# Kernel tuning notes

Measured on AMD Instinct MI355X. Metric: run time of the kernel, lower is better.

## Reference

```python
import jax, jax.numpy as jnp
import numpy as np

B, S, D, DOM, L = 16, 512, 512, 8, 3  # batch, seq_len, mem_dim (S==D required by outputs*rel), domains, layers


def setup_inputs() -> dict:
    key = jax.random.key(0)
    ks = jax.random.split(key, 16)
    adj = jax.random.uniform(ks[0], (B, S, S), jnp.float32)
    rel = jax.random.uniform(ks[1], (B, S, S), jnp.float32)
    gcn_inputs = jax.random.normal(ks[2], (B, S, D), jnp.float32)
    frontrel = jax.random.normal(ks[3], (B, S, D), jnp.float32)
    backrel = jax.random.normal(ks[4], (B, S, D), jnp.float32)
    # depmap: exactly one selected column per (b, row) so masked_select reshapes to [B,S]
    depmap = jax.nn.one_hot(jax.random.randint(ks[5], (B, S), 0, S), S, dtype=jnp.float32)
    dom_idx = jax.random.randint(ks[6], (B, S), 0, DOM)
    has_dom = jax.random.bernoulli(ks[7], 0.5, (B, S)).astype(jnp.float32)
    domain_id = jax.nn.one_hot(dom_idx, DOM, dtype=jnp.float32) * has_dom[..., None]
    redom_idx = jax.random.randint(ks[8], (B, S), 0, DOM)
    has_re = jax.random.bernoulli(ks[9], 0.5, (B, S)).astype(jnp.float32)
    redomain_id = jax.nn.one_hot(redom_idx, DOM, dtype=jnp.float32) * has_re[..., None]
    domain = jax.random.bernoulli(ks[10], 0.5, (B, S, DOM, 1))
    mask = jnp.ones((B, S), dtype=bool)
    sc = 1.0 / np.sqrt(D)
    W_layers = jax.random.normal(ks[11], (L, D, D), jnp.float32) * sc
    b_layers = jnp.zeros((L, D), jnp.float32)
    prelu_a = jnp.full((L,), 0.25, jnp.float32)  # nn.PReLU default
    W_dg = jax.random.normal(ks[12], (D, D), jnp.float32) * sc
    b_dg = jnp.zeros((D,), jnp.float32)
    W_mg = jax.random.normal(ks[13], (2 * D, D), jnp.float32) * (1.0 / np.sqrt(2 * D))
    b_mg = jnp.zeros((D,), jnp.float32)
    W_out = jax.random.normal(ks[14], (L * D, D), jnp.float32) * (1.0 / np.sqrt(L * D))
    b_out = jnp.zeros((D,), jnp.float32)
    return dict(adj=adj, domain=domain, domain_id=domain_id, redomain_id=redomain_id,
                frontrel=frontrel, backrel=backrel, depmap=depmap, rel=rel,
                gcn_inputs=gcn_inputs, mask=mask, W_layers=W_layers, b_layers=b_layers,
                prelu_a=prelu_a, W_dg=W_dg, b_dg=b_dg, W_mg=W_mg, b_mg=b_mg,
                W_out=W_out, b_out=b_out)


def _forward(adj, domain, domain_id, redomain_id, frontrel, backrel, depmap, rel,
             gcn_inputs, W_layers, b_layers, prelu_a, W_dg, b_dg, W_mg, b_mg, W_out, b_out):
    denom = jnp.sum(adj, axis=2, keepdims=True) + 1.0                     # [B,S,1]
    domain_mask = jnp.sum(domain_id, axis=-1, keepdims=True) == 1.0       # [B,S,1]
    redomain_mask = jnp.sum(redomain_id, axis=-1, keepdims=True) == 1.0   # [B,S,1]
    frontadj = jnp.sum(adj * depmap, axis=-1)                             # [B,S]
    backadj = jnp.sum(jnp.swapaxes(adj, -1, -2) * depmap, axis=-1)        # [B,S]
    outputs = gcn_inputs
    outs = []
    for l in range(L):
        frontoutputs = jnp.where(domain_mask, 0.0, outputs)
        backoutputs = jnp.where(redomain_mask, 0.0, jnp.einsum('bij,bjd->bid', rel, outputs))
        # domain pooling: mask then max over sequence -> [B,DOM,D]
        pooled = jnp.max(jnp.where(domain, -10000.0, outputs[:, :, None, :]), axis=1)
        domain_outputs = jax.nn.sigmoid(pooled @ W_dg + b_dg)             # domain_gate
        frontoutputs = frontoutputs + jnp.einsum('bsk,bkd->bsd', domain_id, domain_outputs)
        backoutputs = backoutputs + jnp.einsum('bsk,bkd->bsd', redomain_id, domain_outputs)
        frontdepadj = jax.nn.sigmoid(jnp.concatenate([frontoutputs, frontrel], -1) @ W_mg + b_mg)
        backdepadj = jax.nn.sigmoid(jnp.concatenate([backoutputs, backrel], -1) @ W_mg + b_mg)
        delta = jnp.einsum('bji,bjd->bid', rel, frontadj[..., None] * frontdepadj * frontoutputs)
        delta = delta + backadj[..., None] * backdepadj * backoutputs
        Ax = jnp.einsum('bij,bjd->bid', adj, outputs * rel)               # requires S==D
        AxW = (Ax @ W_layers[l] + b_layers[l]) + (outputs @ W_layers[l] + b_layers[l]) + delta
        x = AxW / denom
        outputs = jnp.where(x >= 0, x, prelu_a[l] * x)                    # PReLU
        outs.append(outputs)                                              # dropout is eval-mode identity
    gcn_outputs = jnp.concatenate(outs, axis=2)                           # [B,S,L*D]
    return gcn_outputs @ W_out + b_out + gcn_inputs


def reference(adj, domain, domain_id, redomain_id, frontrel, backrel, depmap, rel,
              gcn_inputs, mask, W_layers, b_layers, prelu_a, W_dg, b_dg, W_mg, b_mg,
              W_out, b_out):
    return _forward(adj, domain, domain_id, redomain_id, frontrel, backrel, depmap, rel,
                    gcn_inputs, W_layers, b_layers, prelu_a, W_dg, b_dg, W_mg, b_mg,
                    W_out, b_out)
```

## Files before the change

### kernel.cpp

```cpp
#include <hip/hip_runtime.h>
#include <math.h>

#define SD_  (512*512)
#define BSD_ (16*512*512)

typedef unsigned short u16;
typedef short s16x8 __attribute__((ext_vector_type(8)));
typedef float f32x4 __attribute__((ext_vector_type(4)));

__device__ __forceinline__ float sigmoidf_(float x) { return 1.0f / (1.0f + __expf(-x)); }

__device__ __forceinline__ u16 f2bf(float f) {
    unsigned int u = __float_as_uint(f);
    u += 0x7fffu + ((u >> 16) & 1u);
    return (u16)(u >> 16);
}
__device__ __forceinline__ float bf2f(u16 h) { return __uint_as_float((unsigned)h << 16); }

__device__ __forceinline__ void glds16(const void* g, void* l) {
    __builtin_amdgcn_global_load_lds((const __attribute__((address_space(1))) unsigned int*)g,
                                     (__attribute__((address_space(3))) unsigned int*)l, 16, 0, 0);
}

struct GP {
    const u16 *A1, *A2;  int lda1, lda2;  long sA;
    const u16 *B1, *B2;  int ldb1, ldb2;  long sB;
    void *C1, *C2;  int obf1, obf2, ldc1, ldc2;  long sC;
    u16 *CT1, *CT2;  long sCT;
    const void *Ci1, *Ci2;  int cm1, cm2, ldci1, ldci2;  long sCi1, sCi2;
    const float *bias;  float bS;
    const float *sc1, *sc2;
    const int *selm1, *seli1, *selm2, *seli2;
    const float *DG;
    const float *invden, *prelu;  int pidx;
    int M, K, zs, swzX, swzY;
};

template<int EPI, int ASEL>
__global__ __launch_bounds__(512, 6)
void gemm3(const GP p)
{
    __shared__ short LS[24576];
    const int tid = threadIdx.x;
    int bx, by, bz;
    if (p.swzX >= 0) {
        const int bid = blockIdx.x + gridDim.x * (blockIdx.y + gridDim.y * blockIdx.z);
        const int ppx = (gridDim.y * gridDim.z) >> 3;
        const int xcd = bid & 7, idx = bid >> 3;
        const int pair = xcd * ppx + (idx >> p.swzX);
        bx = idx & ((1 << p.swzX) - 1);
        by = pair & ((1 << p.swzY) - 1);
        bz = pair >> p.swzY;
    } else { bx = blockIdx.x; by = blockIdx.y; bz = blockIdx.z; }

    const int seg = (bz >= p.zs) ? 1 : 0;
    const int z = seg ? bz - p.zs : bz;
    const u16* Ab = (seg ? p.A2 : p.A1) + z * p.sA;
    const int lda = seg ? p.lda2 : p.lda1;
    const u16* Bb = (seg ? p.B2 : p.B1) + z * p.sB;
    const int ldb = seg ? p.ldb2 : p.ldb1;

    const int m0 = by * 128, n0 = bx * 64;
    const int srow = ((tid >> 6) << 4) | (tid & 15);
    const int sk0 = ((tid >> 4) & 3) << 3;
    const bool doB = tid < 256;

    const u16* aRow = Ab + (long)(m0 + srow) * lda + sk0;
    const u16* bRow = Bb + (long)(n0 + srow) * ldb + sk0;

    int aselv = 0; long dgo = 0;
    if (ASEL) {
        const int* selm = seg ? p.selm2 : p.selm1;
        const int* seli = seg ? p.seli2 : p.seli1;
        const int r0 = m0 + srow;
        aselv = selm[r0];
        dgo = (long)(((r0 >> 9) << 3) + seli[r0]) * 512 + sk0;
    }

    auto stage = [&](int kk, int buf) {
        short* base = &LS[buf * 6144];
        if (ASEL) {
            s16x8 v;
            if (aselv) {
                const float* dg = p.DG + dgo + kk;
#pragma unroll
                for (int q = 0; q < 8; ++q) v[q] = (short)f2bf(dg[q]);
            } else v = *(const s16x8*)(aRow + kk);
            *(s16x8*)&base[tid * 8] = v;
        } else {
            glds16(aRow + kk, &base[tid * 8]);
        }
        if (doB) glds16(bRow + kk, &base[4096 + tid * 8]);
    };

    const int wave = tid >> 6, lane = tid & 63;
    const int gA = (wave >> 1) << 1;
    const int gB = (wave & 1) << 1;

    f32x4 acc[2][2] = {};
    const int nkb = p.K >> 5;
    stage(0, 0);
    stage(32, 1);
    for (int kb = 0; kb < nkb; ++kb) {
        if (kb + 2 < nkb) stage((kb + 2) << 5, (kb + 2) & 3);
        const int ahead = (nkb - 1 - kb) < 2 ? (nkb - 1 - kb) : 2;
        if (ASEL) {
            if (doB) {
                if (ahead == 2)      asm volatile("s_waitcnt vmcnt(2)" ::: "memory");
                else if (ahead == 1) asm volatile("s_waitcnt vmcnt(1)" ::: "memory");
                else                 asm volatile("s_waitcnt vmcnt(0)" ::: "memory");
            } else {
                asm volatile("s_waitcnt vmcnt(0)" ::: "memory");
            }
            asm volatile("s_waitcnt lgkmcnt(0)" ::: "memory");
        } else {
            if (doB) {
                if (ahead == 2)      asm volatile("s_waitcnt vmcnt(4)" ::: "memory");
                else if (ahead == 1) asm volatile("s_waitcnt vmcnt(2)" ::: "memory");
                else                 asm volatile("s_waitcnt vmcnt(0)" ::: "memory");
            } else {
                if (ahead == 2)      asm volatile("s_waitcnt vmcnt(2)" ::: "memory");
                else if (ahead == 1) asm volatile("s_waitcnt vmcnt(1)" ::: "memory");
                else                 asm volatile("s_waitcnt vmcnt(0)" ::: "memory");
            }
        }
        __builtin_amdgcn_s_barrier();
        const short* ls = &LS[(kb & 3) * 6144];
        s16x8 aF[2], bF[2];
#pragma unroll
        for (int mt = 0; mt < 2; ++mt) aF[mt] = *(const s16x8*)&ls[((gA + mt) * 64 + lane) * 8];
#pragma unroll
        for (int nt = 0; nt < 2; ++nt) bF[nt] = *(const s16x8*)&ls[4096 + ((gB + nt) * 64 + lane) * 8];
#pragma unroll
        for (int mt = 0; mt < 2; ++mt)
#pragma unroll
            for (int nt = 0; nt < 2; ++nt)
                acc[mt][nt] = __builtin_amdgcn_mfma_f32_16x16x32_bf16(aF[mt], bF[nt], acc[mt][nt], 0, 0, 0);
    }

    const int ml = lane & 15, quad = lane >> 4;
    const int wm = (wave >> 1) * 32, wn = (wave & 1) * 32;
    u16* Cb16 = (u16*)(seg ? p.C2 : p.C1);
    float* Cb32 = (float*)(seg ? p.C2 : p.C1);
    const int haveC = (seg ? p.C2 : p.C1) != nullptr;
    const int obf = seg ? p.obf2 : p.obf1;
    const int ldc = seg ? p.ldc2 : p.ldc1;
    if (haveC) { if (obf) Cb16 += z * p.sC; else Cb32 += z * p.sC; }
    u16* CTb = seg ? p.CT2 : p.CT1;
    if (CTb) CTb += z * p.sCT;
    const u16* CiT = (const u16*)(seg ? p.Ci2 : p.Ci1);
    const float* Ci32 = (const float*)(seg ? p.Ci2 : p.Ci1);
    const int cm = seg ? p.cm2 : p.cm1;
    const int ldci = seg ? p.ldci2 : p.ldci1;
    {
        const long sCi = seg ? p.sCi2 : p.sCi1;
        if (cm) CiT += z * sCi; else Ci32 += z * sCi;
    }
    const float pal = (EPI == 4) ? p.prelu[p.pidx] : 0.0f;
    const float* scp = (EPI == 8) ? (seg ? p.sc2 : p.sc1) : nullptr;
    const int* eselm = (EPI == 8) ? (seg ? p.selm2 : p.selm1) : nullptr;
    const int* eseli2 = (EPI == 8) ? (seg ? p.seli2 : p.seli1) : nullptr;

    const bool useEp = haveC && (obf == 1);
    u16* epbuf = (u16*)LS;
    if (useEp) __syncthreads();

#pragma unroll
    for (int mt = 0; mt < 2; ++mt) {
#pragma unroll
        for (int nt = 0; nt < 2; ++nt) {
            const int col = n0 + wn + nt * 16 + ml;
            const int rowb = m0 + wm + mt * 16 + quad * 4;
            float cin4[4];
            if (EPI == 3 || EPI == 4 || EPI == 7 || EPI == 8) {
                if (cm) {
                    const ushort4 c4 = *(const ushort4*)&CiT[(long)(rowb >> 9) * SD_ + (long)col * 512 + (rowb & 511)];
                    cin4[0] = bf2f(c4.x); cin4[1] = bf2f(c4.y); cin4[2] = bf2f(c4.z); cin4[3] = bf2f(c4.w);
                } else {
#pragma unroll
                    for (int r = 0; r < 4; ++r) cin4[r] = Ci32[(long)(rowb + r) * ldci + col];
                }
            }
            u16 pk[4];
#pragma unroll
            for (int r = 0; r < 4; ++r) {
                const int row = rowb + r;
                float x = acc[mt][nt][r];
                if (EPI == 1) x += p.bias[col];
                else if (EPI == 3) x += cin4[r];
                else if (EPI == 4) {
                    x = (x + p.bS * p.bias[col] + cin4[r]) * p.invden[z * p.M + row];
                    x = (x >= 0.0f) ? x : pal * x;
                }
                else if (EPI == 6) x = sigmoidf_(x + p.bias[col]);
                else if (EPI == 7) x += p.bias[col] + cin4[r];
                else if (EPI == 8) {
                    float av;
                    if (eselm[row]) av = p.DG[(long)(((row >> 9) << 3) + eseli2[row]) * 512 + col];
                    else av = bf2f(Ab[(long)row * lda + col]);
                    x = sigmoidf_(x + cin4[r]) * scp[row] * av;
                }
                if (haveC && obf == 0) Cb32[(long)row * ldc + col] = x;
                pk[r] = f2bf(x);
                if (useEp) epbuf[(wm + mt * 16 + quad * 4 + r) * 72 + wn + nt * 16 + ml] = pk[r];
            }
            if (CTb) {
                u16* ct = CTb + (long)(rowb >> 9) * SD_ + (long)col * 512 + (rowb & 511);
                *(ushort4*)ct = *(ushort4*)pk;
            }
        }
    }
    if (useEp) {
        __syncthreads();
        const int lr = tid >> 2, cs = (tid & 3) * 16;
#pragma unroll
        for (int j = 0; j < 2; ++j) {
            const s16x8 v = *(const s16x8*)&epbuf[lr * 72 + cs + j * 8];
            *(s16x8*)&Cb16[(long)(m0 + lr) * ldc + n0 + cs + j * 8] = v;
        }
    }
}

__global__ __launch_bounds__(256)
void cvt_k(const float* __restrict__ s, u16* __restrict__ d)
{
    const long i = ((long)blockIdx.x * 256 + threadIdx.x) * 4;
    const float4 v = *(const float4*)&s[i];
    ushort4 h = { f2bf(v.x), f2bf(v.y), f2bf(v.z), f2bf(v.w) };
    *(ushort4*)&d[i] = h;
}

__global__ __launch_bounds__(256)
void trcvt_k(const float* __restrict__ src, u16* __restrict__ dstT, u16* __restrict__ dstN,
             const int R, const int C, const long sS, const long sDT, const long sDN)
{
    __shared__ u16 t[64][72];
    const float* s = src + blockIdx.z * sS;
    const int r0 = blockIdx.y * 64, c0 = blockIdx.x * 64;
    const int tid = threadIdx.x;
    const int lr = tid >> 2, lc4 = (tid & 3) * 16;
#pragma unroll
    for (int j = 0; j < 4; ++j) {
        const float4 v = *(const float4*)&s[(long)(r0 + lr) * C + c0 + lc4 + j * 4];
        ushort4 h = { f2bf(v.x), f2bf(v.y), f2bf(v.z), f2bf(v.w) };
        *(ushort4*)&t[lr][lc4 + j * 4] = h;
        if (dstN) *(ushort4*)&dstN[blockIdx.z * sDN + (long)(r0 + lr) * C + c0 + lc4 + j * 4] = h;
    }
    __syncthreads();
    const int lcol = tid >> 2, rc = (tid & 3) * 16;
#pragma unroll
    for (int j = 0; j < 2; ++j) {
        s16x8 v;
#pragma unroll
        for (int q = 0; q < 8; ++q) v[q] = (short)t[rc + j * 8 + q][lcol];
        *(s16x8*)&dstT[blockIdx.z * sDT + (long)(c0 + lcol) * R + r0 + rc + j * 8] = v;
    }
}

__global__ __launch_bounds__(256)
void e0_k(const float* __restrict__ adj, const float* __restrict__ depmap,
          const float* __restrict__ domain_id, const float* __restrict__ redomain_id,
          float* __restrict__ invden, float* __restrict__ fa, int* __restrict__ dcol,
          int* __restrict__ dm, int* __restrict__ dsel, int* __restrict__ rm, int* __restrict__ rsel)
{
    const int bs = blockIdx.x;
    const int t = threadIdx.x;
    const float* arow = adj + (long)bs * 512;
    const float* drow = depmap + (long)bs * 512;
    __shared__ float red[256];
    __shared__ int scol;
    if (t == 0) scol = 0;
    const float a0 = arow[t], a1 = arow[t + 256];
    const float p0 = drow[t], p1 = drow[t + 256];
    if (p0 > 0.5f) scol = t;
    if (p1 > 0.5f) scol = t + 256;
    red[t] = a0 + a1;
    __syncthreads();
    for (int off = 128; off > 0; off >>= 1) { if (t < off) red[t] += red[t + off]; __syncthreads(); }
    if (t == 0) invden[bs] = 1.0f / (red[0] + 1.0f);
    __syncthreads();
    red[t] = a0 * p0 + a1 * p1;
    __syncthreads();
    for (int off = 128; off > 0; off >>= 1) { if (t < off) red[t] += red[t + off]; __syncthreads(); }
    if (t == 0) {
        fa[bs] = red[0];
        dcol[bs] = scol;
        const float* q = domain_id + (long)bs * 8;
        float s = 0.f; int sel = 0;
        for (int k = 0; k < 8; ++k) { float v = q[k]; s += v; if (v > 0.5f) sel = k; }
        dm[bs] = (s > 0.5f) ? 1 : 0; dsel[bs] = sel;
        const float* r = redomain_id + (long)bs * 8;
        s = 0.f; sel = 0;
        for (int k = 0; k < 8; ++k) { float v = r[k]; s += v; if (v > 0.5f) sel = k; }
        rm[bs] = (s > 0.5f) ? 1 : 0; rsel[bs] = sel;
    }
}

__global__ void e0b_k(const float* __restrict__ adj, const int* __restrict__ dcol, float* __restrict__ ba)
{
    const int bs = blockIdx.x * 256 + threadIdx.x;
    const int b = bs >> 9, s = bs & 511;
    ba[bs] = adj[((long)b * 512 + dcol[bs]) * 512 + s];
}

__global__ __launch_bounds__(256)
void pool1_k(const u16* __restrict__ OUT, const int ldO, const int* __restrict__ domain,
             const u16* __restrict__ relb, u16* __restrict__ cm, u16* __restrict__ OxRT)
{
    const int b = blockIdx.x >> 4, c = blockIdx.x & 15;
    const int s0 = c * 32, tid = threadIdx.x;
    __shared__ int dom[256];
    dom[tid] = domain[((long)(b * 512 + s0 + (tid >> 3))) * 8 + (tid & 7)];
    __syncthreads();
    const int d0 = tid * 2;
    float mxa[8], mxb[8];
#pragma unroll
    for (int k = 0; k < 8; ++k) { mxa[k] = -10000.0f; mxb[k] = -10000.0f; }
    s16x8 pA[4], pB[4];
#pragma unroll
    for (int s = 0; s < 32; ++s) {
        const int row = b * 512 + s0 + s;
        const unsigned uv = *(const unsigned*)&OUT[(long)row * ldO + d0];
        const unsigned rv = *(const unsigned*)&relb[(long)row * 512 + d0];
        const float vx = bf2f((u16)(uv & 0xffff)), vy = bf2f((u16)(uv >> 16));
        const float rx = bf2f((u16)(rv & 0xffff)), ry = bf2f((u16)(rv >> 16));
        pA[s >> 3][s & 7] = (short)f2bf(vx * rx);
        pB[s >> 3][s & 7] = (short)f2bf(vy * ry);
        const int* ds = &dom[s * 8];
#pragma unroll
        for (int k = 0; k < 8; ++k) {
            mxa[k] = fmaxf(mxa[k], ds[k] ? -10000.0f : vx);
            mxb[k] = fmaxf(mxb[k], ds[k] ? -10000.0f : vy);
        }
    }
#pragma unroll
    for (int j = 0; j < 4; ++j) *(s16x8*)&OxRT[((long)b * 512 + d0) * 512 + s0 + j * 8] = pA[j];
#pragma unroll
    for (int j = 0; j < 4; ++j) *(s16x8*)&OxRT[((long)b * 512 + d0 + 1) * 512 + s0 + j * 8] = pB[j];
#pragma unroll
    for (int k = 0; k < 8; ++k) {
        ushort2 h = { f2bf(mxa[k]), f2bf(mxb[k]) };
        *(ushort2*)&cm[((long)((b * 16 + c) * 8 + k)) * 512 + d0] = h;
    }
}

__global__ void pool2_k(const u16* __restrict__ cm, u16* __restrict__ pooled)
{
    const int q = blockIdx.x * 256 + threadIdx.x;
    const int b = q >> 12, k = (q >> 9) & 7, d = q & 511;
    float m = -1e30f;
    for (int c = 0; c < 16; ++c)
        m = fmaxf(m, bf2f(cm[((long)((b * 16 + c) * 8 + k)) * 512 + d]));
    pooled[((long)(b * 8 + k)) * 512 + d] = f2bf(m);
}

extern "C" void kernel_launch(void* const* d_in, const int* in_sizes, int n_in,
                              void* d_out, int out_size, void* d_ws, size_t ws_size,
                              hipStream_t stream)
{
    const float* adj         = (const float*)d_in[0];
    const int*   domain      = (const int*)d_in[1];
    const float* domain_id   = (const float*)d_in[2];
    const float* redomain_id = (const float*)d_in[3];
    const float* frontrel    = (const float*)d_in[4];
    const float* backrel     = (const float*)d_in[5];
    const float* depmap      = (const float*)d_in[6];
    const float* rel         = (const float*)d_in[7];
    const float* gcn         = (const float*)d_in[8];
    const float* W_layers    = (const float*)d_in[10];
    const float* b_layers    = (const float*)d_in[11];
    const float* prelu_a     = (const float*)d_in[12];
    const float* W_dg        = (const float*)d_in[13];
    const float* b_dg        = (const float*)d_in[14];
    const float* W_mg        = (const float*)d_in[15];
    const float* b_mg        = (const float*)d_in[16];
    const float* W_out       = (const float*)d_in[17];
    const float* b_out       = (const float*)d_in[18];
    float* out = (float*)d_out;

    char* w = (char*)d_ws;
    auto alloc = [&](size_t bytes) { void* p = (void*)w; w += (bytes + 255) & ~(size_t)255; return p; };
    const size_t Bb = (size_t)BSD_ * 2;
    u16* OUTS_bf = (u16*)alloc((size_t)8192 * 1536 * 2);
    u16* OUTT    = (u16*)alloc(Bb);
    u16* gcnT    = (u16*)alloc(Bb);
    u16* RB_bf   = (u16*)alloc(Bb);
    u16* XBT     = (u16*)alloc(Bb);
    u16* XFT     = (u16*)alloc(Bb);
    u16* OxRT    = (u16*)alloc(Bb);
    u16* DLT     = (u16*)alloc(Bb);
    u16* AXO_bf  = (u16*)alloc(Bb);
    u16* BBT     = (u16*)alloc(Bb);
    u16* FBT     = (u16*)alloc(Bb);
    u16* rel_bf  = (u16*)alloc(Bb);
    u16* relT_bf = (u16*)alloc(Bb);
    u16* adj_bf  = (u16*)alloc(Bb);
    u16* gcn_bf  = (u16*)alloc(Bb);
    u16* frel_bf = (u16*)alloc(Bb);
    u16* brel_bf = (u16*)alloc(Bb);
    u16* WmgT1 = (u16*)alloc((size_t)SD_ * 2);
    u16* WmgT2 = (u16*)alloc((size_t)SD_ * 2);
    u16* WdgT  = (u16*)alloc((size_t)SD_ * 2);
    u16* WlT   = (u16*)alloc((size_t)3 * SD_ * 2);
    u16* WoutT = (u16*)alloc((size_t)512 * 1536 * 2);
    u16* cm     = (u16*)alloc((size_t)16 * 16 * 8 * 512 * 2);
    u16* pooled = (u16*)alloc((size_t)16 * 8 * 512 * 2);
    float* DG     = (float*)alloc((size_t)16 * 8 * 512 * 4);
    float* invden = (float*)alloc(8192 * 4);
    float* fa     = (float*)alloc(8192 * 4);
    float* ba     = (float*)alloc(8192 * 4);
    int* dcol = (int*)alloc(8192 * 4);
    int* dm   = (int*)alloc(8192 * 4);
    int* dsel = (int*)alloc(8192 * 4);
    int* rm   = (int*)alloc(8192 * 4);
    int* rsel = (int*)alloc(8192 * 4);

    cvt_k<<<4096, 256, 0, stream>>>(adj, adj_bf);
    cvt_k<<<4096, 256, 0, stream>>>(frontrel, frel_bf);
    cvt_k<<<4096, 256, 0, stream>>>(backrel, brel_bf);
    trcvt_k<<<dim3(8, 8, 16), 256, 0, stream>>>(gcn, gcnT, gcn_bf, 512, 512, SD_, SD_, SD_);
    trcvt_k<<<dim3(8, 8, 16), 256, 0, stream>>>(rel, relT_bf, rel_bf, 512, 512, SD_, SD_, SD_);
    trcvt_k<<<dim3(8, 8, 1), 256, 0, stream>>>(W_mg, WmgT1, nullptr, 512, 512, 0, 0, 0);
    trcvt_k<<<dim3(8, 8, 1), 256, 0, stream>>>(W_mg + SD_, WmgT2, nullptr, 512, 512, 0, 0, 0);
    trcvt_k<<<dim3(8, 8, 1), 256, 0, stream>>>(W_dg, WdgT, nullptr, 512, 512, 0, 0, 0);
    trcvt_k<<<dim3(8, 8, 3), 256, 0, stream>>>(W_layers, WlT, nullptr, 512, 512, SD_, SD_, 0);
    trcvt_k<<<dim3(8, 24, 1), 256, 0, stream>>>(W_out, WoutT, nullptr, 1536, 512, 0, 0, 0);
    e0_k<<<8192, 256, 0, stream>>>(adj, depmap, domain_id, redomain_id, invden, fa, dcol, dm, dsel, rm, rsel);
    e0b_k<<<32, 256, 0, stream>>>(adj, dcol, ba);

    const dim3 blk(512);

    {
        GP p{};
        p.A1 = brel_bf; p.A2 = frel_bf; p.lda1 = p.lda2 = 512; p.sA = 0;
        p.B1 = p.B2 = WmgT2; p.ldb1 = p.ldb2 = 512; p.sB = 0;
        p.CT1 = BBT; p.CT2 = FBT; p.sCT = 0;
        p.bias = b_mg; p.M = 8192; p.K = 512; p.zs = 1; p.swzX = 3; p.swzY = 6;
        gemm3<1, 0><<<dim3(8, 64, 2), blk, 0, stream>>>(p);
    }

    for (int l = 0; l < 3; ++l) {
        const u16* OUTp  = (l == 0) ? gcn_bf : (OUTS_bf + (l - 1) * 512);
        const u16* OUTTp = (l == 0) ? gcnT : OUTT;
        const int ldO = (l == 0) ? 512 : 1536;

        {
            GP p{};
            p.A1 = rel_bf; p.lda1 = 512; p.sA = SD_;
            p.B1 = OUTTp; p.ldb1 = 512; p.sB = SD_;
            p.C1 = RB_bf; p.obf1 = 1; p.ldc1 = 512; p.sC = SD_;
            p.M = 512; p.K = 512; p.zs = 16; p.swzX = 3; p.swzY = 2;
            gemm3<0, 0><<<dim3(8, 4, 16), blk, 0, stream>>>(p);
        }
        pool1_k<<<256, 256, 0, stream>>>(OUTp, ldO, domain, rel_bf, cm, OxRT);
        pool2_k<<<256, 256, 0, stream>>>(cm, pooled);
        {
            GP p{};
            p.A1 = pooled; p.lda1 = 512; p.B1 = WdgT; p.ldb1 = 512;
            p.C1 = DG; p.obf1 = 0; p.ldc1 = 512;
            p.bias = b_dg; p.M = 128; p.K = 512; p.zs = 1; p.swzX = -1;
            gemm3<6, 0><<<dim3(8, 1, 1), blk, 0, stream>>>(p);
        }
        {
            GP p{};
            p.A1 = RB_bf; p.lda1 = 512; p.A2 = OUTp; p.lda2 = ldO; p.sA = 0;
            p.selm1 = rm; p.seli1 = rsel; p.selm2 = dm; p.seli2 = dsel; p.DG = DG;
            p.B1 = p.B2 = WmgT1; p.ldb1 = p.ldb2 = 512; p.sB = 0;
            p.Ci1 = BBT; p.Ci2 = FBT; p.cm1 = p.cm2 = 1; p.ldci1 = p.ldci2 = 512; p.sCi1 = p.sCi2 = 0;
            p.CT1 = XBT; p.CT2 = XFT; p.sCT = 0;
            p.sc1 = ba; p.sc2 = fa; p.M = 8192; p.K = 512; p.zs = 1; p.swzX = 3; p.swzY = 6;
            gemm3<8, 1><<<dim3(8, 64, 2), blk, 0, stream>>>(p);
        }
        {
            GP p{};
            p.A1 = relT_bf; p.lda1 = 512; p.A2 = adj_bf; p.lda2 = 512; p.sA = SD_;
            p.B1 = XFT; p.ldb1 = 512;
            p.B2 = OxRT; p.ldb2 = 512; p.sB = SD_;
            p.Ci1 = XBT; p.cm1 = 1; p.ldci1 = 512; p.sCi1 = SD_;
            p.Ci2 = OUTTp; p.cm2 = 1; p.ldci2 = 512; p.sCi2 = SD_;
            p.CT1 = DLT; p.sCT = SD_;
            p.C2 = AXO_bf; p.obf2 = 1; p.ldc2 = 512; p.sC = SD_;
            p.M = 512; p.K = 512; p.zs = 16; p.swzX = 3; p.swzY = 2;
            gemm3<3, 0><<<dim3(8, 4, 32), blk, 0, stream>>>(p);
        }
        {
            GP p{};
            p.A1 = AXO_bf; p.lda1 = 512; p.sA = SD_;
            p.B1 = WlT + (long)l * SD_; p.ldb1 = 512; p.sB = 0;
            p.Ci1 = DLT; p.cm1 = 1; p.ldci1 = 512; p.sCi1 = SD_;
            p.C1 = OUTS_bf + l * 512; p.obf1 = 1; p.ldc1 = 1536; p.sC = (long)512 * 1536;
            p.CT1 = OUTT; p.sCT = SD_;
            p.bias = b_layers + l * 512; p.bS = 2.0f;
            p.invden = invden; p.prelu = prelu_a; p.pidx = l;
            p.M = 512; p.K = 512; p.zs = 16; p.swzX = 3; p.swzY = 2;
            gemm3<4, 0><<<dim3(8, 4, 16), blk, 0, stream>>>(p);
        }
    }

    {
        GP p{};
        p.A1 = OUTS_bf; p.lda1 = 1536; p.sA = 0;
        p.B1 = WoutT; p.ldb1 = 1536; p.sB = 0;
        p.Ci1 = gcn; p.cm1 = 0; p.ldci1 = 512; p.sCi1 = 0;
        p.C1 = out; p.obf1 = 0; p.ldc1 = 512; p.sC = 0;
        p.bias = b_out; p.M = 8192; p.K = 1536; p.zs = 1; p.swzX = 3; p.swzY = 6;
        gemm3<7, 0><<<dim3(8, 64, 1), blk, 0, stream>>>(p);
    }
}
```

Before: 744.1 us.

## Double K-step per barrier with 3-buffer LDS pipeline in gemm3

The GEMM main loop now processes 64 K-elements per iteration instead of 32, using a 3-stage LDS ring of larger buffers. This halves the number of barriers and waitcnt syncs per tile. All 512 threads now share the B loads instead of only half. The ASEL path loads register data ahead of the barrier and writes it to LDS after, using vectorized float4 reads. In exchange, LDS use per block grows and the occupancy hint drops from 6 to 4 blocks.

```diff
diff --git a/kernel.cpp b/kernel.cpp
--- a/kernel.cpp
+++ b/kernel.cpp
@@ -37,10 +37,10 @@
 };
 
 template<int EPI, int ASEL>
-__global__ __launch_bounds__(512, 6)
+__global__ __launch_bounds__(512, 4)
 void gemm3(const GP p)
 {
-    __shared__ short LS[24576];
+    __shared__ short LS[36864];
     const int tid = threadIdx.x;
     int bx, by, bz;
     if (p.swzX >= 0) {
@@ -63,10 +63,12 @@
     const int m0 = by * 128, n0 = bx * 64;
     const int srow = ((tid >> 6) << 4) | (tid & 15);
     const int sk0 = ((tid >> 4) & 3) << 3;
-    const bool doB = tid < 256;
+    const int srB = (((tid >> 6) & 3) << 4) | (tid & 15);
+    const int skB = (((tid >> 4) & 3) << 3) | ((tid >> 8) << 5);
+    const int bslot = (tid & 255) * 8 + (tid >> 8) * 2048;
 
     const u16* aRow = Ab + (long)(m0 + srow) * lda + sk0;
-    const u16* bRow = Bb + (long)(n0 + srow) * ldb + sk0;
+    const u16* bRow = Bb + (long)(n0 + srB) * ldb + skB;
 
     int aselv = 0; long dgo = 0;
     if (ASEL) {
@@ -77,20 +79,26 @@
         dgo = (long)(((r0 >> 9) << 3) + seli[r0]) * 512 + sk0;
     }
 
-    auto stage = [&](int kk, int buf) {
-        short* base = &LS[buf * 6144];
-        if (ASEL) {
-            s16x8 v;
-            if (aselv) {
-                const float* dg = p.DG + dgo + kk;
-#pragma unroll
-                for (int q = 0; q < 8; ++q) v[q] = (short)f2bf(dg[q]);
-            } else v = *(const s16x8*)(aRow + kk);
-            *(s16x8*)&base[tid * 8] = v;
+    auto stageG = [&](int kb2) {
+        short* base = &LS[(kb2 % 3) * 12288];
+        const int kk = kb2 << 6;
+        glds16(aRow + kk,      &base[tid * 8]);
+        glds16(aRow + kk + 32, &base[4096 + tid * 8]);
+        glds16(bRow + kk,      &base[8192 + bslot]);
+    };
+    auto loadA = [&](int kb2, s16x8& a0, s16x8& a1) {
+        const int kk = kb2 << 6;
+        if (aselv) {
+            const float4* dg = (const float4*)(p.DG + dgo + kk);
+            const float4 d0 = dg[0], d1 = dg[1], d2 = dg[8], d3 = dg[9];
+            a0[0] = (short)f2bf(d0.x); a0[1] = (short)f2bf(d0.y); a0[2] = (short)f2bf(d0.z); a0[3] = (short)f2bf(d0.w);
+            a0[4] = (short)f2bf(d1.x); a0[5] = (short)f2bf(d1.y); a0[6] = (short)f2bf(d1.z); a0[7] = (short)f2bf(d1.w);
+            a1[0] = (short)f2bf(d2.x); a1[1] = (short)f2bf(d2.y); a1[2] = (short)f2bf(d2.z); a1[3] = (short)f2bf(d2.w);
+            a1[4] = (short)f2bf(d3.x); a1[5] = (short)f2bf(d3.y); a1[6] = (short)f2bf(d3.z); a1[7] = (short)f2bf(d3.w);
         } else {
-            glds16(aRow + kk, &base[tid * 8]);
-        }
-        if (doB) glds16(bRow + kk, &base[4096 + tid * 8]);
+            a0 = *(const s16x8*)(aRow + kk);
+            a1 = *(const s16x8*)(aRow + kk + 32);
+        }
     };
 
     const int wave = tid >> 6, lane = tid & 63;
@@ -98,44 +106,58 @@
     const int gB = (wave & 1) << 1;
 
     f32x4 acc[2][2] = {};
-    const int nkb = p.K >> 5;
-    stage(0, 0);
-    stage(32, 1);
+    const int nkb = p.K >> 6;
+
+    if (ASEL) {
+#pragma unroll
+        for (int s = 0; s < 2; ++s) {
+            s16x8 a0, a1;
+            loadA(s, a0, a1);
+            short* base = &LS[s * 12288];
+            *(s16x8*)&base[tid * 8] = a0;
+            *(s16x8*)&base[4096 + tid * 8] = a1;
+            glds16(bRow + (s << 6), &base[8192 + bslot]);
+        }
+    } else { stageG(0); stageG(1); }
+
     for (int kb = 0; kb < nkb; ++kb) {
-        if (kb + 2 < nkb) stage((kb + 2) << 5, (kb + 2) & 3);
-        const int ahead = (nkb - 1 - kb) < 2 ? (nkb - 1 - kb) : 2;
+        s16x8 nA0, nA1;
+        if (ASEL && kb + 2 < nkb) loadA(kb + 2, nA0, nA1);
+
         if (ASEL) {
-            if (doB) {
-                if (ahead == 2)      asm volatile("s_waitcnt vmcnt(2)" ::: "memory");
-                else if (ahead == 1) asm volatile("s_waitcnt vmcnt(1)" ::: "memory");
-                else                 asm volatile("s_waitcnt vmcnt(0)" ::: "memory");
-            } else {
-                asm volatile("s_waitcnt vmcnt(0)" ::: "memory");
-            }
+            if (kb + 2 < nkb)      asm volatile("s_waitcnt vmcnt(3)" ::: "memory");
+            else if (kb + 1 < nkb) asm volatile("s_waitcnt vmcnt(1)" ::: "memory");
+            else                   asm volatile("s_waitcnt vmcnt(0)" ::: "memory");
             asm volatile("s_waitcnt lgkmcnt(0)" ::: "memory");
         } else {
-            if (doB) {
-                if (ahead == 2)      asm volatile("s_waitcnt vmcnt(4)" ::: "memory");
-                else if (ahead == 1) asm volatile("s_waitcnt vmcnt(2)" ::: "memory");
-                else                 asm volatile("s_waitcnt vmcnt(0)" ::: "memory");
-            } else {
-                if (ahead == 2)      asm volatile("s_waitcnt vmcnt(2)" ::: "memory");
-                else if (ahead == 1) asm volatile("s_waitcnt vmcnt(1)" ::: "memory");
-                else                 asm volatile("s_waitcnt vmcnt(0)" ::: "memory");
-            }
+            if (kb + 1 < nkb)      asm volatile("s_waitcnt vmcnt(3)" ::: "memory");
+            else                   asm volatile("s_waitcnt vmcnt(0)" ::: "memory");
         }
         __builtin_amdgcn_s_barrier();
-        const short* ls = &LS[(kb & 3) * 6144];
-        s16x8 aF[2], bF[2];
-#pragma unroll
-        for (int mt = 0; mt < 2; ++mt) aF[mt] = *(const s16x8*)&ls[((gA + mt) * 64 + lane) * 8];
-#pragma unroll
-        for (int nt = 0; nt < 2; ++nt) bF[nt] = *(const s16x8*)&ls[4096 + ((gB + nt) * 64 + lane) * 8];
-#pragma unroll
-        for (int mt = 0; mt < 2; ++mt)
-#pragma unroll
-            for (int nt = 0; nt < 2; ++nt)
-                acc[mt][nt] = __builtin_amdgcn_mfma_f32_16x16x32_bf16(aF[mt], bF[nt], acc[mt][nt], 0, 0, 0);
+
+        if (kb + 2 < nkb) {
+            if (ASEL) {
+                short* base = &LS[((kb + 2) % 3) * 12288];
+                *(s16x8*)&base[tid * 8] = nA0;
+                *(s16x8*)&base[4096 + tid * 8] = nA1;
+                glds16(bRow + ((kb + 2) << 6), &base[8192 + bslot]);
+            } else stageG(kb + 2);
+        }
+
+        const short* ls = &LS[(kb % 3) * 12288];
+#pragma unroll
+        for (int kh = 0; kh < 2; ++kh) {
+            s16x8 aF[2], bF[2];
+#pragma unroll
+            for (int mt = 0; mt < 2; ++mt) aF[mt] = *(const s16x8*)&ls[kh * 4096 + ((gA + mt) * 64 + lane) * 8];
+#pragma unroll
+            for (int nt = 0; nt < 2; ++nt) bF[nt] = *(const s16x8*)&ls[8192 + kh * 2048 + ((gB + nt) * 64 + lane) * 8];
+#pragma unroll
+            for (int mt = 0; mt < 2; ++mt)
+#pragma unroll
+                for (int nt = 0; nt < 2; ++nt)
+                    acc[mt][nt] = __builtin_amdgcn_mfma_f32_16x16x32_bf16(aF[mt], bF[nt], acc[mt][nt], 0, 0, 0);
+        }
     }
 
     const int ml = lane & 15, quad = lane >> 4;
```

Measured after the change: 718.8 us. 3.4% less time.

## Load GEMM fragments directly from global into registers, drop LDS staging

Applied to the files above, without the earlier changes.

Replaces the LDS-staged, async global_load_lds pipeline in the shared GEMM kernel with direct per-lane global loads of MFMA fragments into registers, double-buffered across 64-wide k steps. It also stores the domain-gate result DG in bf16, so the selected-row A loads become plain vector loads without per-element conversion. LDS is kept only for the epilogue buffer, and launch bounds drop to 4 blocks per CU. Because A and B tiles are no longer shared through LDS, each wave reloads data from global/L2 that its neighbours also read, which raises memory traffic and register pressure in exchange for removing barriers and LDS round trips.

```diff
diff --git a/kernel.cpp b/kernel.cpp
--- a/kernel.cpp
+++ b/kernel.cpp
@@ -16,11 +16,6 @@
     return (u16)(u >> 16);
 }
 __device__ __forceinline__ float bf2f(u16 h) { return __uint_as_float((unsigned)h << 16); }
-
-__device__ __forceinline__ void glds16(const void* g, void* l) {
-    __builtin_amdgcn_global_load_lds((const __attribute__((address_space(1))) unsigned int*)g,
-                                     (__attribute__((address_space(3))) unsigned int*)l, 16, 0, 0);
-}
 
 struct GP {
     const u16 *A1, *A2;  int lda1, lda2;  long sA;
@@ -31,16 +26,16 @@
     const float *bias;  float bS;
     const float *sc1, *sc2;
     const int *selm1, *seli1, *selm2, *seli2;
-    const float *DG;
+    const u16 *DG;
     const float *invden, *prelu;  int pidx;
     int M, K, zs, swzX, swzY;
 };
 
 template<int EPI, int ASEL>
-__global__ __launch_bounds__(512, 6)
+__global__ __launch_bounds__(512, 4)
 void gemm3(const GP p)
 {
-    __shared__ short LS[24576];
+    __shared__ u16 epbuf[128 * 72];
     const int tid = threadIdx.x;
     int bx, by, bz;
     if (p.swzX >= 0) {
@@ -61,81 +56,61 @@
     const int ldb = seg ? p.ldb2 : p.ldb1;
 
     const int m0 = by * 128, n0 = bx * 64;
-    const int srow = ((tid >> 6) << 4) | (tid & 15);
-    const int sk0 = ((tid >> 4) & 3) << 3;
-    const bool doB = tid < 256;
-
-    const u16* aRow = Ab + (long)(m0 + srow) * lda + sk0;
-    const u16* bRow = Bb + (long)(n0 + srow) * ldb + sk0;
-
-    int aselv = 0; long dgo = 0;
-    if (ASEL) {
-        const int* selm = seg ? p.selm2 : p.selm1;
-        const int* seli = seg ? p.seli2 : p.seli1;
-        const int r0 = m0 + srow;
-        aselv = selm[r0];
-        dgo = (long)(((r0 >> 9) << 3) + seli[r0]) * 512 + sk0;
-    }
-
-    auto stage = [&](int kk, int buf) {
-        short* base = &LS[buf * 6144];
-        if (ASEL) {
-            s16x8 v;
-            if (aselv) {
-                const float* dg = p.DG + dgo + kk;
-#pragma unroll
-                for (int q = 0; q < 8; ++q) v[q] = (short)f2bf(dg[q]);
-            } else v = *(const s16x8*)(aRow + kk);
-            *(s16x8*)&base[tid * 8] = v;
-        } else {
-            glds16(aRow + kk, &base[tid * 8]);
-        }
-        if (doB) glds16(bRow + kk, &base[4096 + tid * 8]);
-    };
-
     const int wave = tid >> 6, lane = tid & 63;
     const int gA = (wave >> 1) << 1;
     const int gB = (wave & 1) << 1;
+    const int lr = lane & 15, lq = lane >> 4;
+
+    const u16* pAm[2];
+    const u16* pBn[2];
+#pragma unroll
+    for (int mt = 0; mt < 2; ++mt) {
+        const int row = m0 + (gA + mt) * 16 + lr;
+        const u16* base = Ab + (long)row * lda;
+        if (ASEL) {
+            const int* selm = seg ? p.selm2 : p.selm1;
+            const int* seli = seg ? p.seli2 : p.seli1;
+            if (selm[row]) base = p.DG + (long)(((row >> 9) << 3) + seli[row]) * 512;
+        }
+        pAm[mt] = base + lq * 8;
+    }
+#pragma unroll
+    for (int nt = 0; nt < 2; ++nt)
+        pBn[nt] = Bb + (long)(n0 + (gB + nt) * 16 + lr) * ldb + lq * 8;
 
     f32x4 acc[2][2] = {};
-    const int nkb = p.K >> 5;
-    stage(0, 0);
-    stage(32, 1);
-    for (int kb = 0; kb < nkb; ++kb) {
-        if (kb + 2 < nkb) stage((kb + 2) << 5, (kb + 2) & 3);
-        const int ahead = (nkb - 1 - kb) < 2 ? (nkb - 1 - kb) : 2;
-        if (ASEL) {
-            if (doB) {
-                if (ahead == 2)      asm volatile("s_waitcnt vmcnt(2)" ::: "memory");
-                else if (ahead == 1) asm volatile("s_waitcnt vmcnt(1)" ::: "memory");
-                else                 asm volatile("s_waitcnt vmcnt(0)" ::: "memory");
-            } else {
-                asm volatile("s_waitcnt vmcnt(0)" ::: "memory");
-            }
-            asm volatile("s_waitcnt lgkmcnt(0)" ::: "memory");
-        } else {
-            if (doB) {
-                if (ahead == 2)      asm volatile("s_waitcnt vmcnt(4)" ::: "memory");
-                else if (ahead == 1) asm volatile("s_waitcnt vmcnt(2)" ::: "memory");
-                else                 asm volatile("s_waitcnt vmcnt(0)" ::: "memory");
-            } else {
-                if (ahead == 2)      asm volatile("s_waitcnt vmcnt(2)" ::: "memory");
-                else if (ahead == 1) asm volatile("s_waitcnt vmcnt(1)" ::: "memory");
-                else                 asm volatile("s_waitcnt vmcnt(0)" ::: "memory");
-            }
-        }
-        __builtin_amdgcn_s_barrier();
-        const short* ls = &LS[(kb & 3) * 6144];
-        s16x8 aF[2], bF[2];
-#pragma unroll
-        for (int mt = 0; mt < 2; ++mt) aF[mt] = *(const s16x8*)&ls[((gA + mt) * 64 + lane) * 8];
-#pragma unroll
-        for (int nt = 0; nt < 2; ++nt) bF[nt] = *(const s16x8*)&ls[4096 + ((gB + nt) * 64 + lane) * 8];
-#pragma unroll
-        for (int mt = 0; mt < 2; ++mt)
-#pragma unroll
-            for (int nt = 0; nt < 2; ++nt)
-                acc[mt][nt] = __builtin_amdgcn_mfma_f32_16x16x32_bf16(aF[mt], bF[nt], acc[mt][nt], 0, 0, 0);
+
+    auto LD = [&](int kb, s16x8 (&A)[2][2], s16x8 (&B)[2][2]) {
+        const int ko = kb << 6;
+#pragma unroll
+        for (int mt = 0; mt < 2; ++mt) {
+            A[mt][0] = *(const s16x8*)(pAm[mt] + ko);
+            A[mt][1] = *(const s16x8*)(pAm[mt] + ko + 32);
+        }
+#pragma unroll
+        for (int nt = 0; nt < 2; ++nt) {
+            B[nt][0] = *(const s16x8*)(pBn[nt] + ko);
+            B[nt][1] = *(const s16x8*)(pBn[nt] + ko + 32);
+        }
+    };
+    auto MM = [&](const s16x8 (&A)[2][2], const s16x8 (&B)[2][2]) {
+#pragma unroll
+        for (int kh = 0; kh < 2; ++kh)
+#pragma unroll
+            for (int mt = 0; mt < 2; ++mt)
+#pragma unroll
+                for (int nt = 0; nt < 2; ++nt)
+                    acc[mt][nt] = __builtin_amdgcn_mfma_f32_16x16x32_bf16(A[mt][kh], B[nt][kh], acc[mt][nt], 0, 0, 0);
+    };
+
+    const int nkb = p.K >> 6;
+    s16x8 A0[2][2], B0[2][2], A1[2][2], B1[2][2];
+    LD(0, A0, B0);
+    for (int kb = 0; kb < nkb; kb += 2) {
+        LD(kb + 1, A1, B1);
+        MM(A0, B0);
+        if (kb + 2 < nkb) LD(kb + 2, A0, B0);
+        MM(A1, B1);
     }
 
     const int ml = lane & 15, quad = lane >> 4;
@@ -162,8 +137,6 @@
     const int* eseli2 = (EPI == 8) ? (seg ? p.seli2 : p.seli1) : nullptr;
 
     const bool useEp = haveC && (obf == 1);
-    u16* epbuf = (u16*)LS;
-    if (useEp) __syncthreads();
 
 #pragma unroll
     for (int mt = 0; mt < 2; ++mt) {
@@ -196,7 +169,7 @@
                 else if (EPI == 7) x += p.bias[col] + cin4[r];
                 else if (EPI == 8) {
                     float av;
-                    if (eselm[row]) av = p.DG[(long)(((row >> 9) << 3) + eseli2[row]) * 512 + col];
+                    if (eselm[row]) av = bf2f(p.DG[(long)(((row >> 9) << 3) + eseli2[row]) * 512 + col]);
                     else av = bf2f(Ab[(long)row * lda + col]);
                     x = sigmoidf_(x + cin4[r]) * scp[row] * av;
                 }
@@ -212,11 +185,11 @@
     }
     if (useEp) {
         __syncthreads();
-        const int lr = tid >> 2, cs = (tid & 3) * 16;
+        const int lr2 = tid >> 2, cs = (tid & 3) * 16;
 #pragma unroll
         for (int j = 0; j < 2; ++j) {
-            const s16x8 v = *(const s16x8*)&epbuf[lr * 72 + cs + j * 8];
-            *(s16x8*)&Cb16[(long)(m0 + lr) * ldc + n0 + cs + j * 8] = v;
+            const s16x8 v = *(const s16x8*)&epbuf[lr2 * 72 + cs + j * 8];
+            *(s16x8*)&Cb16[(long)(m0 + lr2) * ldc + n0 + cs + j * 8] = v;
         }
     }
 }
@@ -405,7 +378,7 @@
     u16* WoutT = (u16*)alloc((size_t)512 * 1536 * 2);
     u16* cm     = (u16*)alloc((size_t)16 * 16 * 8 * 512 * 2);
     u16* pooled = (u16*)alloc((size_t)16 * 8 * 512 * 2);
-    float* DG     = (float*)alloc((size_t)16 * 8 * 512 * 4);
+    u16* DGb    = (u16*)alloc((size_t)16 * 8 * 512 * 2);
     float* invden = (float*)alloc(8192 * 4);
     float* fa     = (float*)alloc(8192 * 4);
     float* ba     = (float*)alloc(8192 * 4);
@@ -457,14 +430,14 @@
         {
             GP p{};
             p.A1 = pooled; p.lda1 = 512; p.B1 = WdgT; p.ldb1 = 512;
-            p.C1 = DG; p.obf1 = 0; p.ldc1 = 512;
+            p.C1 = DGb; p.obf1 = 1; p.ldc1 = 512;
             p.bias = b_dg; p.M = 128; p.K = 512; p.zs = 1; p.swzX = -1;
             gemm3<6, 0><<<dim3(8, 1, 1), blk, 0, stream>>>(p);
         }
         {
             GP p{};
             p.A1 = RB_bf; p.lda1 = 512; p.A2 = OUTp; p.lda2 = ldO; p.sA = 0;
-            p.selm1 = rm; p.seli1 = rsel; p.selm2 = dm; p.seli2 = dsel; p.DG = DG;
+            p.selm1 = rm; p.seli1 = rsel; p.selm2 = dm; p.seli2 = dsel; p.DG = DGb;
             p.B1 = p.B2 = WmgT1; p.ldb1 = p.ldb2 = 512; p.sB = 0;
             p.Ci1 = BBT; p.Ci2 = FBT; p.cm1 = p.cm2 = 1; p.ldci1 = p.ldci2 = 512; p.sCi1 = p.sCi2 = 0;
             p.CT1 = XBT; p.CT2 = XFT; p.sCT = 0;
```

Result: slower. 1.092 ms (+46.7%).
